# Optimization experiments

Measured on AMD Instinct MI355X. Metric: run time of the kernel, lower is better.

The kernel has to match this reference:

```python
import jax, jax.numpy as jnp
import numpy as np

CH = 64          # channels
OC = 64          # out_channels
B, H, W = 8, 128, 128
NCA_C = CH + OC  # 128, NCA state channels
K = 3            # kernel_size
DILS = (1, 2, 4, 8)
HID = 64         # NCA update hidden
EPS = 1e-5


def setup_inputs() -> dict:
    key = jax.random.key(0)
    ks = jax.random.split(key, 16)
    def n(k, shape, s=0.02):
        return jax.random.normal(k, shape, jnp.float32) * s
    return {
        "x": jax.random.normal(ks[0], (B, H, W, CH), jnp.float32),
        "c": jax.random.normal(ks[1], (B, OC), jnp.float32),
        # Attention params
        "Wq": n(ks[2], (CH, OC)), "bq": jnp.zeros((OC,), jnp.float32),
        "Wk": n(ks[3], (OC, OC)), "bk": jnp.zeros((OC,), jnp.float32),
        "Wv": n(ks[4], (OC, OC)), "bv": jnp.zeros((OC,), jnp.float32),
        "Wo": n(ks[5], (OC, OC)), "bo": jnp.zeros((OC,), jnp.float32),
        "ln_g": jnp.ones((OC,), jnp.float32), "ln_b": jnp.zeros((OC,), jnp.float32),
        # NCA depthwise perception kernels, one per dilation: [4, NCA_C, 1, K, K]
        "pk": n(ks[6], (len(DILS), NCA_C, 1, K, K), 0.1),
        # NCA update MLP
        "W1": n(ks[7], ((1 + len(DILS)) * NCA_C, HID)), "b1": jnp.zeros((HID,), jnp.float32),
        "W2": n(ks[8], (HID, CH)), "b2": jnp.zeros((CH,), jnp.float32),
    }


def _layernorm(z, g, b):
    m = jnp.mean(z, axis=-1, keepdims=True)
    v = jnp.var(z, axis=-1, keepdims=True)
    return (z - m) / jnp.sqrt(v + EPS) * g + b


def _forward(x, c, Wq, bq, Wk, bk, Wv, bv, Wo, bo, ln_g, ln_b, pk, W1, b1, W2, b2):
    b_, h_, w_, _ = x.shape
    # ---- Attention(x, c): single-key softmax pooling over H*W ----
    q = x.reshape(b_, h_ * w_, CH) @ Wq + bq              # [B, HW, OC]
    k = c @ Wk + bk                                        # [B, OC]
    v = c @ Wv + bv                                        # [B, OC]
    scores = jnp.einsum('bno,bo->bn', q, k) * (OC ** -0.5)  # [B, HW]
    attn = jax.nn.softmax(scores, axis=1)                  # softmax over spatial dim
    attended = jnp.einsum('bn,bo->bo', attn, v)            # weighted pool (weights sum to 1)
    a = _layernorm(attended @ Wo + bo + c, ln_g, ln_b)     # out_proj + residual + LN
    c2 = c + a                                             # outer residual in NCAAttention

    # ---- concat broadcast context -> NCA state [B,H,W,NCA_C] ----
    c_exp = jnp.broadcast_to(c2[:, None, None, :], (b_, h_, w_, OC))
    xc = jnp.concatenate([x, c_exp], axis=-1)

    # ---- NCA perception: depthwise dilated convs (SAME padding) ----
    xp = jnp.transpose(xc, (0, 3, 1, 2))                   # NCHW
    feats = [xc]
    for i, d in enumerate(DILS):
        pad = d * (K // 2)
        p = jax.lax.conv_general_dilated(
            xp, pk[i], window_strides=(1, 1),
            padding=[(pad, pad), (pad, pad)], rhs_dilation=(d, d),
            dimension_numbers=('NCHW', 'OIHW', 'NCHW'),
            feature_group_count=NCA_C)
        feats.append(jnp.transpose(p, (0, 2, 3, 1)))
    upd_in = jnp.concatenate(feats, axis=-1)               # [B,H,W,5*NCA_C]

    # ---- NCA update MLP: Linear -> (Dropout=id) -> GELU -> Linear ----
    hidden = jax.nn.gelu(upd_in @ W1 + b1, approximate=False)
    y = hidden @ W2 + b2                                   # [B,H,W,CH]
    # NCA.out_channels (64) != NCA.channels (128) -> no residual add
    return y, c2


def reference(x, c, Wq, bq, Wk, bk, Wv, bv, Wo, bo, ln_g, ln_b, pk, W1, b1, W2, b2):
    return _forward(x, c, Wq, bq, Wk, bk, Wv, bv, Wo, bo, ln_g, ln_b, pk, W1, b1, W2, b2)
```

## Files before the change

### kernel.cpp

```cpp
#include <hip/hip_runtime.h>
#include <hip/hip_bf16.h>
#include <math.h>


typedef float  f32x4 __attribute__((ext_vector_type(4)));
typedef short  s16x8 __attribute__((ext_vector_type(8)));
typedef long   i64x2 __attribute__((ext_vector_type(2)));

static __device__ __forceinline__ unsigned short f2bf(float f) {
    __hip_bfloat16 h = __float2bfloat16(f);
    unsigned short u; __builtin_memcpy(&u, &h, 2); return u;
}
static __device__ __forceinline__ unsigned pk4fp8(float f0, float f1, float f2, float f3) {
    int v = 0;
    v = __builtin_amdgcn_cvt_pk_fp8_f32(f0, f1, v, false);
    v = __builtin_amdgcn_cvt_pk_fp8_f32(f2, f3, v, true);
    return (unsigned)v;
}

#define XROWB  9216
#define XBATCH 1327104
#define USCALE 256.0f

__global__ void prep1(const float* __restrict__ c,
                      const float* __restrict__ Wv, const float* __restrict__ bv,
                      const float* __restrict__ Wo, const float* __restrict__ bo,
                      const float* __restrict__ lng, const float* __restrict__ lnb,
                      float* __restrict__ c2f, float* __restrict__ outc2)
{
    const int b = blockIdx.x, j = threadIdx.x;
    __shared__ float sc[64], sv[64];
    float cj = c[b*64 + j];
    sc[j] = cj; __syncthreads();
    float v = bv[j];
    for (int i = 0; i < 64; ++i) v += sc[i]*Wv[i*64 + j];
    sv[j] = v; __syncthreads();
    float t = bo[j] + cj;
    for (int i = 0; i < 64; ++i) t += sv[i]*Wo[i*64 + j];
    float s = t;
    for (int o = 32; o > 0; o >>= 1) s += __shfl_xor(s, o);
    float m = s * (1.f/64.f);
    float dq = (t - m)*(t - m);
    for (int o = 32; o > 0; o >>= 1) dq += __shfl_xor(dq, o);
    float a = (t - m) / sqrtf(dq*(1.f/64.f) + 1e-5f) * lng[j] + lnb[j];
    float c2 = cj + a;
    c2f[b*64 + j] = c2;
    outc2[b*64 + j] = c2;
}

__global__ void prep2(const float* __restrict__ x,  const float* __restrict__ pk,
                      const float* __restrict__ W1, const float* __restrict__ W2,
                      const float* __restrict__ b1, const float* __restrict__ c2f,
                      unsigned char* __restrict__ xp, unsigned char* __restrict__ Uf,
                      unsigned short* __restrict__ W2s, float* __restrict__ V,
                      float* __restrict__ hc2g, float* __restrict__ CyG,
                      float* __restrict__ CxG)
{
    const int blk = blockIdx.x, tid = threadIdx.x;
    if (blk < 512) {
        int i = blk*256 + tid;
        int xc = i & 127, y = (i >> 7) & 127, b = i >> 14;
        const float* src = x + (size_t)i*64;
        float4 f[16];
        #pragma unroll
        for (int k = 0; k < 16; ++k) f[k] = *(const float4*)(src + k*4);
        unsigned P[16];
        #pragma unroll
        for (int k = 0; k < 16; ++k) P[k] = pk4fp8(f[k].x, f[k].y, f[k].z, f[k].w);
        unsigned char* d = xp + (size_t)b*XBATCH + (size_t)(y+8)*XROWB + (size_t)(xc+8)*64;
        *(uint4*)(d +  0) = make_uint4(P[0], P[1], P[8],  P[9]);
        *(uint4*)(d + 16) = make_uint4(P[2], P[3], P[10], P[11]);
        *(uint4*)(d + 32) = make_uint4(P[4], P[5], P[12], P[13]);
        *(uint4*)(d + 48) = make_uint4(P[6], P[7], P[14], P[15]);
    } else if (blk < 648) {
        int idx = (blk - 512)*256 + tid;
        int b = idx / 4352, r = idx - b*4352;
        int yy, xx;
        if (r < 2304) { int ry = r / 144; xx = r - ry*144; yy = (ry < 8) ? ry : 128 + ry; }
        else { int r2 = r - 2304; yy = 8 + (r2 >> 4); int xi = r2 & 15; xx = (xi < 8) ? xi : 128 + xi; }
        unsigned char* d = xp + (size_t)b*XBATCH + (size_t)yy*XROWB + (size_t)xx*64;
        uint4 z = make_uint4(0,0,0,0);
        *(uint4*)(d) = z; *(uint4*)(d+16) = z; *(uint4*)(d+32) = z; *(uint4*)(d+48) = z;
    } else if (blk < 681) {
        int idx = (blk - 648)*256 + tid;
        if (idx < 8448) {
            int lane = idx & 63, nt = (idx >> 6) & 3, pos = idx >> 8;
            int n  = nt*16 + (lane & 15);
            static constexpr int DI[33] = {3,3,3, 2,2,2, 1,1,1, 0,0,0, -1, 0,0, 1,1, 2,2, 3,3,
                                           0,0,0, 1,1,1, 2,2,2, 3,3,3};
            static constexpr int TT[33] = {0,1,2, 0,1,2, 0,1,2, 0,1,2, 4, 3,5, 3,5, 3,5, 3,5,
                                           6,7,8, 6,7,8, 6,7,8, 6,7,8};
            int di = DI[pos], t = TT[pos];
            float vv[16];
            #pragma unroll
            for (int kc2 = 0; kc2 < 2; ++kc2)
                #pragma unroll
                for (int j = 0; j < 8; ++j) {
                    int ch = kc2*32 + (lane >> 4)*8 + j;
                    float v;
                    if (di < 0) {
                        v = W1[ch*64 + n];
                        for (int dd = 0; dd < 4; ++dd)
                            v += pk[(dd*128 + ch)*9 + 4] * W1[((1+dd)*128 + ch)*64 + n];
                    } else {
                        v = pk[(di*128 + ch)*9 + t] * W1[((1+di)*128 + ch)*64 + n];
                    }
                    vv[kc2*8 + j] = v * USCALE;
                }
            uint4 o;
            o.x = pk4fp8(vv[0],  vv[1],  vv[2],  vv[3]);
            o.y = pk4fp8(vv[4],  vv[5],  vv[6],  vv[7]);
            o.z = pk4fp8(vv[8],  vv[9],  vv[10], vv[11]);
            o.w = pk4fp8(vv[12], vv[13], vv[14], vv[15]);
            *(uint4*)(Uf + (size_t)idx*16) = o;
        }
    } else if (blk < 683) {
        int idx = (blk - 681)*256 + tid;
        int lane = idx & 63, nt = (idx >> 6) & 3, kc2 = (idx >> 8) & 1;
        int n  = nt*16 + (lane & 15);
        int k0 = kc2*32 + (lane >> 4)*8;
        unsigned short e[8];
        #pragma unroll
        for (int j = 0; j < 8; ++j) e[j] = f2bf(W2[(k0+j)*64 + n]);
        uint4 o;
        o.x = (unsigned)e[0] | ((unsigned)e[1] << 16);
        o.y = (unsigned)e[2] | ((unsigned)e[3] << 16);
        o.z = (unsigned)e[4] | ((unsigned)e[5] << 16);
        o.w = (unsigned)e[6] | ((unsigned)e[7] << 16);
        *(uint4*)(W2s + (size_t)idx*8) = o;
    } else if (blk < 755) {
        int idx = (blk - 683)*256 + tid;
        int n = idx & 63, q = idx >> 6;
        int p = q % 36, b = q / 36;
        int di = p/9, t = p%9;
        float s = 0.f;
        for (int j = 0; j < 64; ++j)
            s += c2f[b*64 + j] * pk[(di*128 + 64 + j)*9 + t] * W1[((1+di)*128 + 64 + j)*64 + n];
        V[(size_t)q*64 + n] = s;
    } else if (blk < 757) {
        int idx = (blk - 755)*256 + tid;
        if (idx < 512) {
            int b = idx >> 6, n = idx & 63;
            float s = b1[n];
            for (int j = 0; j < 64; ++j) {
                float wsum = W1[(64 + j)*64 + n];
                for (int di = 0; di < 4; ++di) {
                    float ks = 0.f;
                    for (int t = 0; t < 9; ++t) ks += pk[(di*128 + 64 + j)*9 + t];
                    wsum += ks * W1[((1+di)*128 + 64 + j)*64 + n];
                }
                s += c2f[b*64 + j] * wsum;
            }
            hc2g[idx] = s;
        }
    } else if (blk < 1013) {
        int idx = (blk - 757)*256 + tid;
        int n = idx & 63, y = (idx >> 6) & 127, b = idx >> 13;
        float s = 0.f;
        for (int di = 0; di < 4; ++di) {
            int d = 1 << di;
            int dyo = (y < d) ? 0 : ((y >= 128 - d) ? 2 : -1);
            if (dyo >= 0) {
                for (int j = 0; j < 64; ++j) {
                    float pks = pk[(di*128 + 64 + j)*9 + dyo*3 + 0]
                              + pk[(di*128 + 64 + j)*9 + dyo*3 + 1]
                              + pk[(di*128 + 64 + j)*9 + dyo*3 + 2];
                    s += c2f[b*64 + j] * pks * W1[((1+di)*128 + 64 + j)*64 + n];
                }
            }
        }
        CyG[idx] = s;
    } else {
        int idx = (blk - 1013)*256 + tid;
        int n = idx & 63, xi = (idx >> 6) & 15, b = idx >> 10;
        int xx = (xi < 8) ? xi : 112 + xi;
        float s = 0.f;
        for (int di = 0; di < 4; ++di) {
            int d = 1 << di;
            int dxo = (xx < d) ? 0 : ((xx >= 128 - d) ? 2 : -1);
            if (dxo >= 0) {
                for (int j = 0; j < 64; ++j) {
                    float pks = pk[(di*128 + 64 + j)*9 + 0*3 + dxo]
                              + pk[(di*128 + 64 + j)*9 + 1*3 + dxo]
                              + pk[(di*128 + 64 + j)*9 + 2*3 + dxo];
                    s += c2f[b*64 + j] * pks * W1[((1+di)*128 + 64 + j)*64 + n];
                }
            }
        }
        CxG[idx] = s;
    }
}

#define HID_S 72

__global__ __launch_bounds__(128, 4) void nca_main(
    const unsigned char* __restrict__ xp,
    const unsigned char* __restrict__ U,
    const unsigned short* __restrict__ W2s,
    const float* __restrict__ V,
    const float* __restrict__ hc2g,
    const float* __restrict__ CyG,
    const float* __restrict__ CxG,
    const float* __restrict__ b2,
    float* __restrict__ out)
{
    __shared__ unsigned short hid[64*HID_S];

    const int tid = threadIdx.x;
    const int blk = blockIdx.x;
    const int b  = blk & 7;
    const int q  = blk >> 3;
    const int y  = q >> 1;
    const int xw = (q & 1) * 64;

    const int lane = tid & 63;
    const int w    = tid >> 6;
    const int ln15 = lane & 15;
    const int oct  = lane >> 4;

    const unsigned char* abase = xp + (size_t)b*XBATCH + (size_t)(y + 8)*XROWB
                               + (size_t)(xw + ln15 + 8)*64 + oct*16;
    const unsigned char* ubase = U + (size_t)w*2048 + (size_t)lane*16;

    f32x4 acc[4][2];
    #pragma unroll
    for (int mt = 0; mt < 4; ++mt)
        #pragma unroll
        for (int j = 0; j < 2; ++j) {
            acc[mt][j][0] = 0.f; acc[mt][j][1] = 0.f;
            acc[mt][j][2] = 0.f; acc[mt][j][3] = 0.f;
        }

    static constexpr int OFF[33] = {
        (-8*144-8)*64, (-8*144)*64, (-8*144+8)*64,
        (-4*144-4)*64, (-4*144)*64, (-4*144+4)*64,
        (-2*144-2)*64, (-2*144)*64, (-2*144+2)*64,
        (-1*144-1)*64, (-1*144)*64, (-1*144+1)*64,
        0,
        -64, 64, -128, 128, -256, 256, -512, 512,
        ( 1*144-1)*64, ( 1*144)*64, ( 1*144+1)*64,
        ( 2*144-2)*64, ( 2*144)*64, ( 2*144+2)*64,
        ( 4*144-4)*64, ( 4*144)*64, ( 4*144+4)*64,
        ( 8*144-8)*64, ( 8*144)*64, ( 8*144+8)*64
    };

    i64x2 A0[4], A1[4], B0[2], B1[2];
    auto loadA = [&](i64x2* A, int pos) {
        const unsigned char* rp = abase + OFF[pos];
        #pragma unroll
        for (int mt = 0; mt < 4; ++mt) A[mt] = *(const i64x2*)(rp + mt*1024);
    };
    auto loadB = [&](i64x2* Bv, int pos) {
        const unsigned char* up = ubase + (size_t)pos*4096;
        Bv[0] = *(const i64x2*)(up);
        Bv[1] = *(const i64x2*)(up + 1024);
    };
    auto mfblk = [&](i64x2* A, i64x2* Bv) {
        #pragma unroll
        for (int kc2 = 0; kc2 < 2; ++kc2)
            #pragma unroll
            for (int j = 0; j < 2; ++j) {
                long bf = Bv[j][kc2];
                #pragma unroll
                for (int mt = 0; mt < 4; ++mt)
                    acc[mt][j] = __builtin_amdgcn_mfma_f32_16x16x32_fp8_fp8(A[mt][kc2], bf, acc[mt][j], 0, 0, 0);
            }
    };

    loadA(A0, 0);  loadB(B0, 0);
    loadA(A1, 1);  loadB(B1, 1);

    #pragma unroll 1
    for (int i = 0; i < 16; ++i) {
        mfblk(A0, B0);
        int pa = 2*i + 2;
        loadA(A0, pa); loadB(B0, pa);
        mfblk(A1, B1);
        int pb = (2*i + 3 <= 32) ? (2*i + 3) : 32;
        loadA(A1, pb); loadB(B1, pb);
    }
    mfblk(A0, B0);

    const bool yedge = (y < 8) || (y >= 120);
    #pragma unroll
    for (int j = 0; j < 2; ++j) {
        const int n = (w*2 + j)*16 + ln15;
        const float h0 = hc2g[b*64 + n] - CyG[((b << 7) + y)*64 + n];
        #pragma unroll
        for (int mt = 0; mt < 4; ++mt) {
            #pragma unroll
            for (int r = 0; r < 4; ++r) {
                int m = mt*16 + oct*4 + r;
                int x = xw + m;
                float h = acc[mt][j][r]*(1.0f/USCALE) + h0;
                if (x < 8 || x >= 120) {
                    int xi = (x < 8) ? x : (x - 112);
                    h -= CxG[((b << 4) + xi)*64 + n];
                    if (yedge) {
                        #pragma unroll
                        for (int di = 0; di < 4; ++di) {
                            int d = 1 << di;
                            int dyo = (y < d) ? 0 : ((y >= 128 - d) ? 2 : -1);
                            int dxo = (x < d) ? 0 : ((x >= 128 - d) ? 2 : -1);
                            if (dyo >= 0 && dxo >= 0)
                                h += V[((size_t)b*36 + di*9 + dyo*3 + dxo)*64 + n];
                        }
                    }
                }
                float u = 0.7978845608028654f * (h + 0.044715f*h*h*h);
                float g = h / (1.f + __expf(-2.f*u));
                hid[m*HID_S + n] = f2bf(g);
            }
        }
    }
    __syncthreads();

    f32x4 acc2[4][2];
    #pragma unroll
    for (int mt = 0; mt < 4; ++mt)
        #pragma unroll
        for (int j = 0; j < 2; ++j) {
            acc2[mt][j][0] = 0.f; acc2[mt][j][1] = 0.f;
            acc2[mt][j][2] = 0.f; acc2[mt][j][3] = 0.f;
        }
    #pragma unroll
    for (int kc2 = 0; kc2 < 2; ++kc2) {
        s16x8 a2[4];
        #pragma unroll
        for (int mt = 0; mt < 4; ++mt)
            a2[mt] = *(const s16x8*)&hid[(mt*16 + ln15)*HID_S + kc2*32 + oct*8];
        #pragma unroll
        for (int j = 0; j < 2; ++j) {
            int nt = w*2 + j;
            s16x8 bf = *(const s16x8*)(W2s + ((size_t)(kc2*4 + nt)*64 + lane)*8);
            #pragma unroll
            for (int mt = 0; mt < 4; ++mt)
                acc2[mt][j] = __builtin_amdgcn_mfma_f32_16x16x32_bf16(a2[mt], bf, acc2[mt][j], 0, 0, 0);
        }
    }

    float* ob = out + ((size_t)(b*128 + y))*128*64;
    #pragma unroll
    for (int j = 0; j < 2; ++j) {
        const int n = (w*2 + j)*16 + ln15;
        const float b2v = b2[n];
        #pragma unroll
        for (int mt = 0; mt < 4; ++mt) {
            #pragma unroll
            for (int r = 0; r < 4; ++r) {
                int x = xw + mt*16 + oct*4 + r;
                ob[(size_t)x*64 + n] = acc2[mt][j][r] + b2v;
            }
        }
    }
}

extern "C" void kernel_launch(void* const* d_in, const int* in_sizes, int n_in,
                              void* d_out, int out_size, void* d_ws, size_t ws_size,
                              hipStream_t stream) {
    const float* x   = (const float*)d_in[0];
    const float* c   = (const float*)d_in[1];
    const float* Wv  = (const float*)d_in[6];
    const float* bv  = (const float*)d_in[7];
    const float* Wo  = (const float*)d_in[8];
    const float* bo  = (const float*)d_in[9];
    const float* lng = (const float*)d_in[10];
    const float* lnb = (const float*)d_in[11];
    const float* pk  = (const float*)d_in[12];
    const float* W1  = (const float*)d_in[13];
    const float* b1  = (const float*)d_in[14];
    const float* W2  = (const float*)d_in[15];
    const float* b2  = (const float*)d_in[16];
    float* out = (float*)d_out;

    char* w = (char*)d_ws;
    unsigned char*  xpb  = (unsigned char*)(w);
    unsigned char*  Uf   = (unsigned char*)(w + 10616832);
    unsigned short* W2s  = (unsigned short*)(w + 10752000);
    float*          V    = (float*)         (w + 10760192);
    float*          hc2g = (float*)         (w + 10833920);
    float*          c2f  = (float*)         (w + 10835968);
    float*          CyG  = (float*)         (w + 10838016);
    float*          CxG  = (float*)         (w + 11100160);

    prep1<<<8, 64, 0, stream>>>(c, Wv, bv, Wo, bo, lng, lnb, c2f, out + 8388608);
    prep2<<<1045, 256, 0, stream>>>(x, pk, W1, W2, b1, c2f, xpb, Uf, W2s, V, hc2g, CyG, CxG);
    nca_main<<<2048, 128, 0, stream>>>(xpb, Uf, W2s, V, hc2g, CyG, CxG, b2, out);
}
```

Before: 182.2 us.

## Use scaled fp8 16x16x128 MFMA, merge prep kernels, widen main blocks

The main conv-as-GEMM loop moves from 16x16x32 fp8 MFMA to the gfx950 mfma_scale 16x16x128 f8f6f4 instruction. Two stencil positions are packed into each K=128 step, and U is re-laid-out to match. Each 256-thread block now covers two rows with each wave owning all 64 output columns, so the second GEMM needs no block-wide sync. The two prep kernels are merged into one: each block that needs c2 recomputes it in shared memory, and CyG storage shrinks to edge rows only. This removes a launch and halves the MFMA instruction count, at the cost of more registers and redundant c2 computation.

```diff
diff --git a/kernel.cpp b/kernel.cpp
--- a/kernel.cpp
+++ b/kernel.cpp
@@ -3,9 +3,9 @@
 #include <math.h>
 
 
-typedef float  f32x4 __attribute__((ext_vector_type(4)));
-typedef short  s16x8 __attribute__((ext_vector_type(8)));
-typedef long   i64x2 __attribute__((ext_vector_type(2)));
+typedef float f32x4 __attribute__((ext_vector_type(4)));
+typedef short s16x8 __attribute__((ext_vector_type(8)));
+typedef int   v8i   __attribute__((ext_vector_type(8)));
 
 static __device__ __forceinline__ unsigned short f2bf(float f) {
     __hip_bfloat16 h = __float2bfloat16(f);
@@ -22,56 +22,73 @@
 #define XBATCH 1327104
 #define USCALE 256.0f
 
-__global__ void prep1(const float* __restrict__ c,
-                      const float* __restrict__ Wv, const float* __restrict__ bv,
-                      const float* __restrict__ Wo, const float* __restrict__ bo,
-                      const float* __restrict__ lng, const float* __restrict__ lnb,
-                      float* __restrict__ c2f, float* __restrict__ outc2)
+__device__ __constant__ int DIc[33] = {3,3,3, 2,2,2, 1,1,1, 0,0,0, -1, 0,0, 1,1, 2,2, 3,3,
+                                       0,0,0, 1,1,1, 2,2,2, 3,3,3};
+__device__ __constant__ int TTc[33] = {0,1,2, 0,1,2, 0,1,2, 0,1,2, 4, 3,5, 3,5, 3,5, 3,5,
+                                       6,7,8, 6,7,8, 6,7,8, 6,7,8};
+
+static __device__ void c2_block(int b, int tid,
+    const float* __restrict__ c,  const float* __restrict__ Wv,
+    const float* __restrict__ bv, const float* __restrict__ Wo,
+    const float* __restrict__ bo, const float* __restrict__ lng,
+    const float* __restrict__ lnb, float* sc2)
 {
-    const int b = blockIdx.x, j = threadIdx.x;
-    __shared__ float sc[64], sv[64];
-    float cj = c[b*64 + j];
-    sc[j] = cj; __syncthreads();
-    float v = bv[j];
-    for (int i = 0; i < 64; ++i) v += sc[i]*Wv[i*64 + j];
-    sv[j] = v; __syncthreads();
-    float t = bo[j] + cj;
-    for (int i = 0; i < 64; ++i) t += sv[i]*Wo[i*64 + j];
-    float s = t;
-    for (int o = 32; o > 0; o >>= 1) s += __shfl_xor(s, o);
-    float m = s * (1.f/64.f);
-    float dq = (t - m)*(t - m);
-    for (int o = 32; o > 0; o >>= 1) dq += __shfl_xor(dq, o);
-    float a = (t - m) / sqrtf(dq*(1.f/64.f) + 1e-5f) * lng[j] + lnb[j];
-    float c2 = cj + a;
-    c2f[b*64 + j] = c2;
-    outc2[b*64 + j] = c2;
-}
-
-__global__ void prep2(const float* __restrict__ x,  const float* __restrict__ pk,
-                      const float* __restrict__ W1, const float* __restrict__ W2,
-                      const float* __restrict__ b1, const float* __restrict__ c2f,
-                      unsigned char* __restrict__ xp, unsigned char* __restrict__ Uf,
-                      unsigned short* __restrict__ W2s, float* __restrict__ V,
-                      float* __restrict__ hc2g, float* __restrict__ CyG,
-                      float* __restrict__ CxG)
+    __shared__ float vsh[64], tsh[64];
+    if (tid < 64) sc2[tid] = c[b*64 + tid];
+    __syncthreads();
+    if (tid < 64) {
+        float v = bv[tid];
+        for (int i = 0; i < 64; ++i) v += sc2[i]*Wv[i*64 + tid];
+        vsh[tid] = v;
+    }
+    __syncthreads();
+    if (tid < 64) {
+        float t = bo[tid] + sc2[tid];
+        for (int i = 0; i < 64; ++i) t += vsh[i]*Wo[i*64 + tid];
+        tsh[tid] = t;
+    }
+    __syncthreads();
+    if (tid < 64) {
+        float m = 0.f;
+        for (int i = 0; i < 64; ++i) m += tsh[i];
+        m *= (1.f/64.f);
+        float vv = 0.f;
+        for (int i = 0; i < 64; ++i) { float d = tsh[i] - m; vv += d*d; }
+        vv *= (1.f/64.f);
+        float a = (tsh[tid] - m) / sqrtf(vv + 1e-5f) * lng[tid] + lnb[tid];
+        sc2[tid] = sc2[tid] + a;
+    }
+    __syncthreads();
+}
+
+__global__ void prep(const float* __restrict__ x,  const float* __restrict__ c,
+                     const float* __restrict__ Wv, const float* __restrict__ bv,
+                     const float* __restrict__ Wo, const float* __restrict__ bo,
+                     const float* __restrict__ lng,const float* __restrict__ lnb,
+                     const float* __restrict__ pk, const float* __restrict__ W1,
+                     const float* __restrict__ W2, const float* __restrict__ b1,
+                     unsigned char* __restrict__ xp, unsigned char* __restrict__ Uf,
+                     unsigned short* __restrict__ W2s, float* __restrict__ V,
+                     float* __restrict__ hc2g, float* __restrict__ CyGe,
+                     float* __restrict__ CxG, float* __restrict__ outc2)
 {
     const int blk = blockIdx.x, tid = threadIdx.x;
+    __shared__ float c2s[64];
     if (blk < 512) {
         int i = blk*256 + tid;
         int xc = i & 127, y = (i >> 7) & 127, b = i >> 14;
         const float* src = x + (size_t)i*64;
-        float4 f[16];
-        #pragma unroll
-        for (int k = 0; k < 16; ++k) f[k] = *(const float4*)(src + k*4);
         unsigned P[16];
         #pragma unroll
-        for (int k = 0; k < 16; ++k) P[k] = pk4fp8(f[k].x, f[k].y, f[k].z, f[k].w);
+        for (int k = 0; k < 16; ++k) {
+            float4 f = *(const float4*)(src + k*4);
+            P[k] = pk4fp8(f.x, f.y, f.z, f.w);
+        }
         unsigned char* d = xp + (size_t)b*XBATCH + (size_t)(y+8)*XROWB + (size_t)(xc+8)*64;
-        *(uint4*)(d +  0) = make_uint4(P[0], P[1], P[8],  P[9]);
-        *(uint4*)(d + 16) = make_uint4(P[2], P[3], P[10], P[11]);
-        *(uint4*)(d + 32) = make_uint4(P[4], P[5], P[12], P[13]);
-        *(uint4*)(d + 48) = make_uint4(P[6], P[7], P[14], P[15]);
+        *(uint4*)(d +  0) = make_uint4(P[0],  P[1],  P[2],  P[3]);
+        *(uint4*)(d + 16) = make_uint4(P[4],  P[5],  P[6],  P[7]);
+        *(uint4*)(d + 32) = make_uint4(P[8],  P[9],  P[10], P[11]);
+        *(uint4*)(d + 48) = make_uint4(P[12], P[13], P[14], P[15]);
     } else if (blk < 648) {
         int idx = (blk - 512)*256 + tid;
         int b = idx / 4352, r = idx - b*4352;
@@ -81,41 +98,42 @@
         unsigned char* d = xp + (size_t)b*XBATCH + (size_t)yy*XROWB + (size_t)xx*64;
         uint4 z = make_uint4(0,0,0,0);
         *(uint4*)(d) = z; *(uint4*)(d+16) = z; *(uint4*)(d+32) = z; *(uint4*)(d+48) = z;
-    } else if (blk < 681) {
+    } else if (blk < 665) {
         int idx = (blk - 648)*256 + tid;
-        if (idx < 8448) {
-            int lane = idx & 63, nt = (idx >> 6) & 3, pos = idx >> 8;
-            int n  = nt*16 + (lane & 15);
-            static constexpr int DI[33] = {3,3,3, 2,2,2, 1,1,1, 0,0,0, -1, 0,0, 1,1, 2,2, 3,3,
-                                           0,0,0, 1,1,1, 2,2,2, 3,3,3};
-            static constexpr int TT[33] = {0,1,2, 0,1,2, 0,1,2, 0,1,2, 4, 3,5, 3,5, 3,5, 3,5,
-                                           6,7,8, 6,7,8, 6,7,8, 6,7,8};
-            int di = DI[pos], t = TT[pos];
-            float vv[16];
-            #pragma unroll
-            for (int kc2 = 0; kc2 < 2; ++kc2)
-                #pragma unroll
-                for (int j = 0; j < 8; ++j) {
-                    int ch = kc2*32 + (lane >> 4)*8 + j;
-                    float v;
-                    if (di < 0) {
-                        v = W1[ch*64 + n];
-                        for (int dd = 0; dd < 4; ++dd)
-                            v += pk[(dd*128 + ch)*9 + 4] * W1[((1+dd)*128 + ch)*64 + n];
-                    } else {
-                        v = pk[(di*128 + ch)*9 + t] * W1[((1+di)*128 + ch)*64 + n];
-                    }
-                    vv[kc2*8 + j] = v * USCALE;
+        int lane = idx & 63, nt = (idx >> 6) & 3, pair = idx >> 8;
+        int n   = nt*16 + (lane & 15);
+        int oct = lane >> 4;
+        int pos = pair*2 + (oct >> 1);
+        int chh = (oct & 1)*32;
+        unsigned Pw[8];
+        if (pos > 32) {
+            #pragma unroll
+            for (int q = 0; q < 8; ++q) Pw[q] = 0u;
+        } else {
+            int di = DIc[pos], t = TTc[pos];
+            float vv[32];
+            #pragma unroll
+            for (int j = 0; j < 32; ++j) {
+                int ch = chh + j;
+                float v;
+                if (di < 0) {
+                    v = W1[ch*64 + n];
+                    for (int dd = 0; dd < 4; ++dd)
+                        v += pk[(dd*128 + ch)*9 + 4] * W1[((1+dd)*128 + ch)*64 + n];
+                } else {
+                    v = pk[(di*128 + ch)*9 + t] * W1[((1+di)*128 + ch)*64 + n];
                 }
-            uint4 o;
-            o.x = pk4fp8(vv[0],  vv[1],  vv[2],  vv[3]);
-            o.y = pk4fp8(vv[4],  vv[5],  vv[6],  vv[7]);
-            o.z = pk4fp8(vv[8],  vv[9],  vv[10], vv[11]);
-            o.w = pk4fp8(vv[12], vv[13], vv[14], vv[15]);
-            *(uint4*)(Uf + (size_t)idx*16) = o;
-        }
-    } else if (blk < 683) {
-        int idx = (blk - 681)*256 + tid;
+                vv[j] = v * USCALE;
+            }
+            #pragma unroll
+            for (int q = 0; q < 8; ++q)
+                Pw[q] = pk4fp8(vv[q*4], vv[q*4+1], vv[q*4+2], vv[q*4+3]);
+        }
+        uint4* d = (uint4*)(Uf + (size_t)idx*32);
+        d[0] = make_uint4(Pw[0], Pw[1], Pw[2], Pw[3]);
+        d[1] = make_uint4(Pw[4], Pw[5], Pw[6], Pw[7]);
+    } else if (blk < 667) {
+        int idx = (blk - 665)*256 + tid;
         int lane = idx & 63, nt = (idx >> 6) & 3, kc2 = (idx >> 8) & 1;
         int n  = nt*16 + (lane & 15);
         int k0 = kc2*32 + (lane >> 4)*8;
@@ -128,19 +146,22 @@
         o.z = (unsigned)e[4] | ((unsigned)e[5] << 16);
         o.w = (unsigned)e[6] | ((unsigned)e[7] << 16);
         *(uint4*)(W2s + (size_t)idx*8) = o;
-    } else if (blk < 755) {
-        int idx = (blk - 683)*256 + tid;
-        int n = idx & 63, q = idx >> 6;
-        int p = q % 36, b = q / 36;
+    } else if (blk < 739) {
+        int blkl = blk - 667;
+        int b = blkl / 9;
+        c2_block(b, tid, c, Wv, bv, Wo, bo, lng, lnb, c2s);
+        int idx = (blkl % 9)*256 + tid;
+        int p = idx >> 6, n = idx & 63;
         int di = p/9, t = p%9;
         float s = 0.f;
         for (int j = 0; j < 64; ++j)
-            s += c2f[b*64 + j] * pk[(di*128 + 64 + j)*9 + t] * W1[((1+di)*128 + 64 + j)*64 + n];
-        V[(size_t)q*64 + n] = s;
-    } else if (blk < 757) {
-        int idx = (blk - 755)*256 + tid;
-        if (idx < 512) {
-            int b = idx >> 6, n = idx & 63;
+            s += c2s[j] * pk[(di*128 + 64 + j)*9 + t] * W1[((1+di)*128 + 64 + j)*64 + n];
+        V[((size_t)b*36 + p)*64 + n] = s;
+    } else if (blk < 747) {
+        int b = blk - 739;
+        c2_block(b, tid, c, Wv, bv, Wo, bo, lng, lnb, c2s);
+        if (tid < 64) {
+            int n = tid;
             float s = b1[n];
             for (int j = 0; j < 64; ++j) {
                 float wsum = W1[(64 + j)*64 + n];
@@ -149,13 +170,18 @@
                     for (int t = 0; t < 9; ++t) ks += pk[(di*128 + 64 + j)*9 + t];
                     wsum += ks * W1[((1+di)*128 + 64 + j)*64 + n];
                 }
-                s += c2f[b*64 + j] * wsum;
-            }
-            hc2g[idx] = s;
-        }
-    } else if (blk < 1013) {
-        int idx = (blk - 757)*256 + tid;
-        int n = idx & 63, y = (idx >> 6) & 127, b = idx >> 13;
+                s += c2s[j] * wsum;
+            }
+            hc2g[b*64 + n] = s;
+            outc2[b*64 + n] = c2s[n];
+        }
+    } else if (blk < 779) {
+        int blkl = blk - 747;
+        int b = blkl / 4;
+        c2_block(b, tid, c, Wv, bv, Wo, bo, lng, lnb, c2s);
+        int idx = (blkl % 4)*256 + tid;
+        int yi = idx >> 6, n = idx & 63;
+        int y = (yi < 8) ? yi : 112 + yi;
         float s = 0.f;
         for (int di = 0; di < 4; ++di) {
             int d = 1 << di;
@@ -165,14 +191,17 @@
                     float pks = pk[(di*128 + 64 + j)*9 + dyo*3 + 0]
                               + pk[(di*128 + 64 + j)*9 + dyo*3 + 1]
                               + pk[(di*128 + 64 + j)*9 + dyo*3 + 2];
-                    s += c2f[b*64 + j] * pks * W1[((1+di)*128 + 64 + j)*64 + n];
+                    s += c2s[j] * pks * W1[((1+di)*128 + 64 + j)*64 + n];
                 }
             }
         }
-        CyG[idx] = s;
+        CyGe[((b << 4) + yi)*64 + n] = s;
     } else {
-        int idx = (blk - 1013)*256 + tid;
-        int n = idx & 63, xi = (idx >> 6) & 15, b = idx >> 10;
+        int blkl = blk - 779;
+        int b = blkl / 4;
+        c2_block(b, tid, c, Wv, bv, Wo, bo, lng, lnb, c2s);
+        int idx = (blkl % 4)*256 + tid;
+        int xi = idx >> 6, n = idx & 63;
         int xx = (xi < 8) ? xi : 112 + xi;
         float s = 0.f;
         for (int di = 0; di < 4; ++di) {
@@ -183,55 +212,56 @@
                     float pks = pk[(di*128 + 64 + j)*9 + 0*3 + dxo]
                               + pk[(di*128 + 64 + j)*9 + 1*3 + dxo]
                               + pk[(di*128 + 64 + j)*9 + 2*3 + dxo];
-                    s += c2f[b*64 + j] * pks * W1[((1+di)*128 + 64 + j)*64 + n];
+                    s += c2s[j] * pks * W1[((1+di)*128 + 64 + j)*64 + n];
                 }
             }
         }
-        CxG[idx] = s;
+        CxG[((b << 4) + xi)*64 + n] = s;
     }
 }
 
 #define HID_S 72
 
-__global__ __launch_bounds__(128, 4) void nca_main(
+__global__ __launch_bounds__(256) void nca_main(
     const unsigned char* __restrict__ xp,
     const unsigned char* __restrict__ U,
     const unsigned short* __restrict__ W2s,
     const float* __restrict__ V,
     const float* __restrict__ hc2g,
-    const float* __restrict__ CyG,
+    const float* __restrict__ CyGe,
     const float* __restrict__ CxG,
     const float* __restrict__ b2,
     float* __restrict__ out)
 {
-    __shared__ unsigned short hid[64*HID_S];
+    __shared__ unsigned short hid[256*HID_S];
 
     const int tid = threadIdx.x;
     const int blk = blockIdx.x;
     const int b  = blk & 7;
-    const int q  = blk >> 3;
-    const int y  = q >> 1;
-    const int xw = (q & 1) * 64;
+    const int y0 = (blk >> 3) * 2;
 
     const int lane = tid & 63;
     const int w    = tid >> 6;
+    const int y    = y0 + (w >> 1);
+    const int xw   = (w & 1) * 64;
     const int ln15 = lane & 15;
     const int oct  = lane >> 4;
+    const int hi   = oct >> 1;
 
     const unsigned char* abase = xp + (size_t)b*XBATCH + (size_t)(y + 8)*XROWB
-                               + (size_t)(xw + ln15 + 8)*64 + oct*16;
-    const unsigned char* ubase = U + (size_t)w*2048 + (size_t)lane*16;
-
-    f32x4 acc[4][2];
+                               + (size_t)(xw + ln15 + 8)*64 + (oct & 1)*32;
+    const unsigned char* ubase = U + (size_t)lane*32;
+
+    f32x4 acc[4][4];
     #pragma unroll
     for (int mt = 0; mt < 4; ++mt)
         #pragma unroll
-        for (int j = 0; j < 2; ++j) {
-            acc[mt][j][0] = 0.f; acc[mt][j][1] = 0.f;
-            acc[mt][j][2] = 0.f; acc[mt][j][3] = 0.f;
-        }
-
-    static constexpr int OFF[33] = {
+        for (int nt = 0; nt < 4; ++nt) {
+            acc[mt][nt][0] = 0.f; acc[mt][nt][1] = 0.f;
+            acc[mt][nt][2] = 0.f; acc[mt][nt][3] = 0.f;
+        }
+
+    static constexpr int OFF[34] = {
         (-8*144-8)*64, (-8*144)*64, (-8*144+8)*64,
         (-4*144-4)*64, (-4*144)*64, (-4*144+4)*64,
         (-2*144-2)*64, (-2*144)*64, (-2*144+2)*64,
@@ -241,58 +271,60 @@
         ( 1*144-1)*64, ( 1*144)*64, ( 1*144+1)*64,
         ( 2*144-2)*64, ( 2*144)*64, ( 2*144+2)*64,
         ( 4*144-4)*64, ( 4*144)*64, ( 4*144+4)*64,
-        ( 8*144-8)*64, ( 8*144)*64, ( 8*144+8)*64
+        ( 8*144-8)*64, ( 8*144)*64, ( 8*144+8)*64,
+        0
     };
 
-    i64x2 A0[4], A1[4], B0[2], B1[2];
-    auto loadA = [&](i64x2* A, int pos) {
-        const unsigned char* rp = abase + OFF[pos];
-        #pragma unroll
-        for (int mt = 0; mt < 4; ++mt) A[mt] = *(const i64x2*)(rp + mt*1024);
+    v8i A0[4], A1[4], B0[4], B1[4];
+    auto loadAB = [&](v8i* A, v8i* B, int P) {
+        int off = hi ? OFF[2*P + 1] : OFF[2*P];
+        const unsigned char* rp = abase + off;
+        #pragma unroll
+        for (int mt = 0; mt < 4; ++mt) A[mt] = *(const v8i*)(rp + mt*1024);
+        const unsigned char* up = ubase + (size_t)P*8192;
+        #pragma unroll
+        for (int nt = 0; nt < 4; ++nt) B[nt] = *(const v8i*)(up + nt*2048);
     };
-    auto loadB = [&](i64x2* Bv, int pos) {
-        const unsigned char* up = ubase + (size_t)pos*4096;
-        Bv[0] = *(const i64x2*)(up);
-        Bv[1] = *(const i64x2*)(up + 1024);
+    auto mfblk = [&](v8i* A, v8i* B) {
+        #pragma unroll
+        for (int nt = 0; nt < 4; ++nt)
+            #pragma unroll
+            for (int mt = 0; mt < 4; ++mt)
+                acc[mt][nt] = __builtin_amdgcn_mfma_scale_f32_16x16x128_f8f6f4(
+                    A[mt], B[nt], acc[mt][nt], 0, 0, 0, 127, 0, 127);
     };
-    auto mfblk = [&](i64x2* A, i64x2* Bv) {
-        #pragma unroll
-        for (int kc2 = 0; kc2 < 2; ++kc2)
-            #pragma unroll
-            for (int j = 0; j < 2; ++j) {
-                long bf = Bv[j][kc2];
-                #pragma unroll
-                for (int mt = 0; mt < 4; ++mt)
-                    acc[mt][j] = __builtin_amdgcn_mfma_f32_16x16x32_fp8_fp8(A[mt][kc2], bf, acc[mt][j], 0, 0, 0);
-            }
-    };
-
-    loadA(A0, 0);  loadB(B0, 0);
-    loadA(A1, 1);  loadB(B1, 1);
-
+
+    loadAB(A0, B0, 0);
+    loadAB(A1, B1, 1);
     #pragma unroll 1
-    for (int i = 0; i < 16; ++i) {
+    for (int i = 0; i < 8; ++i) {
         mfblk(A0, B0);
         int pa = 2*i + 2;
-        loadA(A0, pa); loadB(B0, pa);
+        loadAB(A0, B0, pa);
         mfblk(A1, B1);
-        int pb = (2*i + 3 <= 32) ? (2*i + 3) : 32;
-        loadA(A1, pb); loadB(B1, pb);
+        int pb = (2*i + 3 <= 16) ? (2*i + 3) : 16;
+        loadAB(A1, B1, pb);
     }
     mfblk(A0, B0);
 
     const bool yedge = (y < 8) || (y >= 120);
-    #pragma unroll
-    for (int j = 0; j < 2; ++j) {
-        const int n = (w*2 + j)*16 + ln15;
-        const float h0 = hc2g[b*64 + n] - CyG[((b << 7) + y)*64 + n];
-        #pragma unroll
-        for (int mt = 0; mt < 4; ++mt) {
+    const int  yi    = (y < 8) ? y : (y - 112);
+    float hcv[4];
+    #pragma unroll
+    for (int nt = 0; nt < 4; ++nt) {
+        const int n = nt*16 + ln15;
+        hcv[nt] = hc2g[b*64 + n] - (yedge ? CyGe[((b << 4) + yi)*64 + n] : 0.f);
+    }
+    #pragma unroll
+    for (int mt = 0; mt < 4; ++mt) {
+        #pragma unroll
+        for (int nt = 0; nt < 4; ++nt) {
+            const int n = nt*16 + ln15;
             #pragma unroll
             for (int r = 0; r < 4; ++r) {
                 int m = mt*16 + oct*4 + r;
                 int x = xw + m;
-                float h = acc[mt][j][r]*(1.0f/USCALE) + h0;
+                float h = acc[mt][nt][r]*(1.0f/USCALE) + hcv[nt];
                 if (x < 8 || x >= 120) {
                     int xi = (x < 8) ? x : (x - 112);
                     h -= CxG[((b << 4) + xi)*64 + n];
@@ -309,47 +341,44 @@
                 }
                 float u = 0.7978845608028654f * (h + 0.044715f*h*h*h);
                 float g = h / (1.f + __expf(-2.f*u));
-                hid[m*HID_S + n] = f2bf(g);
-            }
-        }
-    }
-    __syncthreads();
-
-    f32x4 acc2[4][2];
+                hid[(w*64 + m)*HID_S + n] = f2bf(g);
+            }
+        }
+    }
+
+    f32x4 acc2[4][4];
     #pragma unroll
     for (int mt = 0; mt < 4; ++mt)
         #pragma unroll
-        for (int j = 0; j < 2; ++j) {
-            acc2[mt][j][0] = 0.f; acc2[mt][j][1] = 0.f;
-            acc2[mt][j][2] = 0.f; acc2[mt][j][3] = 0.f;
+        for (int nt = 0; nt < 4; ++nt) {
+            acc2[mt][nt][0] = 0.f; acc2[mt][nt][1] = 0.f;
+            acc2[mt][nt][2] = 0.f; acc2[mt][nt][3] = 0.f;
         }
     #pragma unroll
     for (int kc2 = 0; kc2 < 2; ++kc2) {
         s16x8 a2[4];
         #pragma unroll
         for (int mt = 0; mt < 4; ++mt)
-            a2[mt] = *(const s16x8*)&hid[(mt*16 + ln15)*HID_S + kc2*32 + oct*8];
-        #pragma unroll
-        for (int j = 0; j < 2; ++j) {
-            int nt = w*2 + j;
+            a2[mt] = *(const s16x8*)&hid[(w*64 + mt*16 + ln15)*HID_S + kc2*32 + oct*8];
+        #pragma unroll
+        for (int nt = 0; nt < 4; ++nt) {
             s16x8 bf = *(const s16x8*)(W2s + ((size_t)(kc2*4 + nt)*64 + lane)*8);
             #pragma unroll
             for (int mt = 0; mt < 4; ++mt)
-                acc2[mt][j] = __builtin_amdgcn_mfma_f32_16x16x32_bf16(a2[mt], bf, acc2[mt][j], 0, 0, 0);
+                acc2[mt][nt] = __builtin_amdgcn_mfma_f32_16x16x32_bf16(a2[mt], bf, acc2[mt][nt], 0, 0, 0);
         }
     }
 
     float* ob = out + ((size_t)(b*128 + y))*128*64;
     #pragma unroll
-    for (int j = 0; j < 2; ++j) {
-        const int n = (w*2 + j)*16 + ln15;
-        const float b2v = b2[n];
+    for (int nt = 0; nt < 4; ++nt) {
+        const float b2v = b2[nt*16 + ln15];
         #pragma unroll
         for (int mt = 0; mt < 4; ++mt) {
             #pragma unroll
             for (int r = 0; r < 4; ++r) {
                 int x = xw + mt*16 + oct*4 + r;
-                ob[(size_t)x*64 + n] = acc2[mt][j][r] + b2v;
+                ob[(size_t)x*64 + nt*16 + ln15] = acc2[mt][nt][r] + b2v;
             }
         }
     }
@@ -376,14 +405,13 @@
     char* w = (char*)d_ws;
     unsigned char*  xpb  = (unsigned char*)(w);
     unsigned char*  Uf   = (unsigned char*)(w + 10616832);
-    unsigned short* W2s  = (unsigned short*)(w + 10752000);
-    float*          V    = (float*)         (w + 10760192);
-    float*          hc2g = (float*)         (w + 10833920);
-    float*          c2f  = (float*)         (w + 10835968);
-    float*          CyG  = (float*)         (w + 10838016);
-    float*          CxG  = (float*)         (w + 11100160);
-
-    prep1<<<8, 64, 0, stream>>>(c, Wv, bv, Wo, bo, lng, lnb, c2f, out + 8388608);
-    prep2<<<1045, 256, 0, stream>>>(x, pk, W1, W2, b1, c2f, xpb, Uf, W2s, V, hc2g, CyG, CxG);
-    nca_main<<<2048, 128, 0, stream>>>(xpb, Uf, W2s, V, hc2g, CyG, CxG, b2, out);
-}
+    unsigned short* W2s  = (unsigned short*)(w + 10756096);
+    float*          V    = (float*)         (w + 10764288);
+    float*          hc2g = (float*)         (w + 10838016);
+    float*          CyGe = (float*)         (w + 10840064);
+    float*          CxG  = (float*)         (w + 10872832);
+
+    prep<<<811, 256, 0, stream>>>(x, c, Wv, bv, Wo, bo, lng, lnb, pk, W1, W2, b1,
+                                  xpb, Uf, W2s, V, hc2g, CyGe, CxG, out + 8388608);
+    nca_main<<<512, 256, 0, stream>>>(xpb, Uf, W2s, V, hc2g, CyGe, CxG, b2, out);
+}
```

Measured after the change: 197.4 us. 8.3% more time.
